# Kernel tuning notes

Hardware: AMD Instinct MI355X
Metric: run time of the kernel (lower is better)

## Reference

```python
import jax, jax.numpy as jnp
import numpy as np

NUM_GROUPS = 32
EPS = 1e-5


def setup_inputs() -> dict:
    key = jax.random.key(0)
    ks = jax.random.split(key, 3)
    B, C, H, W = 4, 256, 64, 64
    x = jax.random.normal(ks[0], (B, C, H, W), dtype=jnp.float32)
    gn_w = jnp.ones((C,), dtype=jnp.float32)
    gn_b = jnp.zeros((C,), dtype=jnp.float32)
    qkv_w = jax.random.normal(ks[1], (3 * C, C), dtype=jnp.float32) * (C ** -0.5)
    qkv_b = jnp.zeros((3 * C,), dtype=jnp.float32)
    proj_w = jax.random.normal(ks[2], (C, C), dtype=jnp.float32) * (C ** -0.5)
    proj_b = jnp.zeros((C,), dtype=jnp.float32)
    return {"x": x, "gn_w": gn_w, "gn_b": gn_b, "qkv_w": qkv_w,
            "qkv_b": qkv_b, "proj_w": proj_w, "proj_b": proj_b}


def group_norm(x, w, b):
    B, C, H, W = x.shape
    xg = x.reshape(B, NUM_GROUPS, C // NUM_GROUPS, H, W)
    mu = xg.mean(axis=(2, 3, 4), keepdims=True)
    var = xg.var(axis=(2, 3, 4), keepdims=True)
    xn = ((xg - mu) * jax.lax.rsqrt(var + EPS)).reshape(B, C, H, W)
    return xn * w[None, :, None, None] + b[None, :, None, None]


def reference(x, gn_w, gn_b, qkv_w, qkv_b, proj_w, proj_b):
    B, C, H, W = x.shape
    h = group_norm(x, gn_w, gn_b)
    # 1x1 conv == per-pixel matmul over channels
    qkv = jnp.einsum('oc,bchw->bohw', qkv_w, h) + qkv_b[None, :, None, None]
    q, k, v = jnp.split(qkv, 3, axis=1)          # each [B, C, H, W]
    q = q.reshape(B, C, H * W).transpose(0, 2, 1)  # [B, N, C]
    k = k.reshape(B, C, H * W)                     # [B, C, N]
    v = v.reshape(B, C, H * W).transpose(0, 2, 1)  # [B, N, C]
    attn = jnp.einsum('bnc,bcm->bnm', q, k) * (C ** -0.5)
    attn = jax.nn.softmax(attn, axis=-1)
    h = jnp.einsum('bnm,bmc->bnc', attn, v)        # [B, N, C]
    h = h.transpose(0, 2, 1).reshape(B, C, H, W)
    out = jnp.einsum('oc,bchw->bohw', proj_w, h) + proj_b[None, :, None, None]
    return x + out
```

## Files before the change

### kernel.cpp

```cpp
#include <hip/hip_runtime.h>
#include <hip/hip_bf16.h>

#define DEVI __device__ __forceinline__

typedef short bf16x8 __attribute__((ext_vector_type(8)));
typedef float f32x4  __attribute__((ext_vector_type(4)));
typedef float f32x16 __attribute__((ext_vector_type(16)));
typedef unsigned short u16;
typedef unsigned int u32;

using bf16 = __hip_bfloat16;

DEVI bf16x8 ld8(const bf16* p) { return *reinterpret_cast<const bf16x8*>(p); }

DEVI u16 f2bu(float f) {
  union { bf16 h; u16 u; } c; c.h = __float2bfloat16(f); return c.u;
}
DEVI float b2f(u16 u) {
  union { float f; unsigned int i; } c; c.i = ((unsigned int)u) << 16; return c.f;
}

DEVI void gload_lds16(const bf16* g, bf16* l) {
  typedef const __attribute__((address_space(1))) char* gp_t;
  typedef __attribute__((address_space(3))) char* lp_t;
  __builtin_amdgcn_global_load_lds((gp_t)(const void*)g, (lp_t)(void*)l, 16, 0, 0);
}

#define MFMA16(a, b, c) __builtin_amdgcn_mfma_f32_16x16x32_bf16((a), (b), (c), 0, 0, 0)
#define MFMA32(a, b, c) __builtin_amdgcn_mfma_f32_32x32x16_bf16((a), (b), (c), 0, 0, 0)


__global__ __launch_bounds__(256) void wconv_kernel(const float* __restrict__ wq,
                                                    const float* __restrict__ wp,
                                                    bf16* __restrict__ wqb,
                                                    bf16* __restrict__ wpb) {
  int tid = blockIdx.x * 256 + threadIdx.x;
  const bool isq = tid < 49152;
  float4 v = isq ? ((const float4*)wq)[tid] : ((const float4*)wp)[tid - 49152];
  alignas(8) bf16 o[4] = { __float2bfloat16(v.x), __float2bfloat16(v.y),
                           __float2bfloat16(v.z), __float2bfloat16(v.w) };
  uint2 pk = *reinterpret_cast<uint2*>(o);
  if (isq) ((uint2*)wqb)[tid] = pk;
  else     ((uint2*)wpb)[tid - 49152] = pk;
}

__global__ __launch_bounds__(256) void gn_kernel(const float* __restrict__ x,
                                                 const float* __restrict__ gw,
                                                 const float* __restrict__ gb,
                                                 bf16* __restrict__ ht) {
  const int blk = blockIdx.x;
  const int bb = blk >> 5, g = blk & 31;
  const float* xg = x + (size_t)(bb * 256 + g * 8) * 4096;

  float s = 0.f, ss = 0.f;
  const float4* x4 = (const float4*)xg;
  for (int i = threadIdx.x; i < 8192; i += 256) {
    float4 v = x4[i];
    s  += v.x + v.y + v.z + v.w;
    ss += v.x * v.x + v.y * v.y + v.z * v.z + v.w * v.w;
  }
  #pragma unroll
  for (int off = 32; off; off >>= 1) {
    s  += __shfl_down(s, off);
    ss += __shfl_down(ss, off);
  }
  __shared__ float red[8];
  int wave = threadIdx.x >> 6;
  if ((threadIdx.x & 63) == 0) { red[wave * 2] = s; red[wave * 2 + 1] = ss; }
  __syncthreads();
  if (threadIdx.x == 0) {
    float S = red[0] + red[2] + red[4] + red[6];
    float SS = red[1] + red[3] + red[5] + red[7];
    float mu = S * (1.f / 32768.f);
    float var = SS * (1.f / 32768.f) - mu * mu;
    red[0] = mu; red[1] = rsqrtf(var + 1e-5f);
  }
  __syncthreads();
  const float mu = red[0], rstd = red[1];

  float gm[8], bt[8];
  #pragma unroll
  for (int j = 0; j < 8; ++j) {
    float wv = gw[g * 8 + j] * rstd;
    gm[j] = wv; bt[j] = gb[g * 8 + j] - mu * wv;
  }
  bf16* hrow = ht + (size_t)bb * 4096 * 256 + g * 8;
  for (int n = threadIdx.x; n < 4096; n += 256) {
    alignas(16) u16 u[8];
    #pragma unroll
    for (int j = 0; j < 8; ++j)
      u[j] = f2bu(xg[j * 4096 + n] * gm[j] + bt[j]);
    *reinterpret_cast<uint4*>(hrow + (size_t)n * 256) = *reinterpret_cast<uint4*>(u);
  }
}

__global__ __launch_bounds__(256, 2) void qkv_gemm(const bf16* __restrict__ ht,
                                                   const bf16* __restrict__ wq,
                                                   const float* __restrict__ qkvb,
                                                   bf16* __restrict__ qkvt) {
  const int phys = blockIdx.x;
  const int L = (phys & 7) * 96 + (phys >> 3);
  const int bb = L / 192; const int rem = L - bb * 192;
  const int nt = rem / 6, ot = rem - nt * 6;

  const int tid = threadIdx.x, lane = tid & 63, w = tid >> 6;
  const int ln = lane & 15, hi = lane >> 4;
  const int wr = w >> 1, wc = w & 1;
  const int n_base = nt * 128, o_base = ot * 128;
  const bf16* hb = ht + (size_t)bb * 4096 * 256;

  __shared__ bf16 At[2][128 * 64];
  __shared__ bf16 Bt[2][128 * 64];

  f32x4 acc[4][4] = {};

  {
    #pragma unroll
    for (int i = 0; i < 4; ++i) {
      int G = i * 256 + tid; int row = G >> 3, g = G & 7;
      int cofs = (g ^ (row & 7)) << 3;
      gload_lds16(hb + (size_t)(n_base + row) * 256 + cofs, At[0] + (size_t)G * 8);
      gload_lds16(wq + (size_t)(o_base + row) * 256 + cofs, Bt[0] + (size_t)G * 8);
    }
  }
  __syncthreads();

  int cur = 0;
  for (int ks = 0; ks < 4; ++ks) {
    if (ks < 3) {
      int k0 = (ks + 1) * 64;
      #pragma unroll
      for (int i = 0; i < 4; ++i) {
        int G = i * 256 + tid; int row = G >> 3, g = G & 7;
        int cofs = k0 + ((g ^ (row & 7)) << 3);
        gload_lds16(hb + (size_t)(n_base + row) * 256 + cofs, At[cur ^ 1] + (size_t)G * 8);
        gload_lds16(wq + (size_t)(o_base + row) * 256 + cofs, Bt[cur ^ 1] + (size_t)G * 8);
      }
    }
    const char* Ab = (const char*)At[cur];
    const char* Bb = (const char*)Bt[cur];
    __builtin_amdgcn_s_setprio(1);
    #pragma unroll
    for (int cb = 0; cb < 2; ++cb) {
      bf16x8 af[4], bfr[4];
      #pragma unroll
      for (int i = 0; i < 4; ++i) {
        int row = wr * 64 + i * 16 + ln;
        af[i] = *(const bf16x8*)(Ab + row * 128 + (((cb * 4 + hi) ^ (row & 7)) << 4));
      }
      #pragma unroll
      for (int j = 0; j < 4; ++j) {
        int row = wc * 64 + j * 16 + ln;
        bfr[j] = *(const bf16x8*)(Bb + row * 128 + (((cb * 4 + hi) ^ (row & 7)) << 4));
      }
      #pragma unroll
      for (int i = 0; i < 4; ++i)
        #pragma unroll
        for (int j = 0; j < 4; ++j)
          acc[i][j] = MFMA16(af[i], bfr[j], acc[i][j]);
    }
    __builtin_amdgcn_s_setprio(0);
    __syncthreads();
    cur ^= 1;
  }

  const float sc = (ot < 2) ? 0.0625f : 1.0f;
  bf16* ob = qkvt + (size_t)bb * 4096 * 768;
  #pragma unroll
  for (int j = 0; j < 4; ++j) {
    int o = o_base + wc * 64 + j * 16 + ln;
    float bias = qkvb[o];
    #pragma unroll
    for (int i = 0; i < 4; ++i)
      #pragma unroll
      for (int r = 0; r < 4; ++r) {
        int n = n_base + wr * 64 + i * 16 + hi * 4 + r;
        ob[(size_t)n * 768 + o] = __float2bfloat16((acc[i][j][r] + bias) * sc);
      }
  }
}

__global__ __launch_bounds__(256) void vtrans_kernel(const bf16* __restrict__ qkvt,
                                                     bf16* __restrict__ vT) {
  int bid = blockIdx.x;
  int ct = bid & 3, ntile = (bid >> 2) & 63, bb = bid >> 8;
  __shared__ bf16 T[64][72];
  int tid = threadIdx.x;
  int i = tid >> 3, j8 = (tid & 7) * 8;
  const bf16* src = qkvt + (size_t)bb * 4096 * 768 + (size_t)(ntile * 64 + i) * 768 + 512 + ct * 64 + j8;
  #pragma unroll
  for (int p = 0; p < 2; ++p) {
    bf16x8 v = ld8(src + (size_t)p * 32 * 768);
    *reinterpret_cast<bf16x8*>(&T[i + p * 32][j8]) = v;
  }
  __syncthreads();
  bf16* dst = vT + (size_t)bb * 256 * 4096 + (size_t)(ct * 64) * 4096 + ntile * 64;
  #pragma unroll
  for (int p = 0; p < 2; ++p) {
    int c = i + p * 32;
    alignas(16) bf16 u[8];
    #pragma unroll
    for (int q = 0; q < 8; ++q) u[q] = T[j8 + q][c];
    *reinterpret_cast<uint4*>(dst + (size_t)c * 4096 + j8) = *reinterpret_cast<uint4*>(u);
  }
}

__global__ __launch_bounds__(256, 2) void attn_kernel(const bf16* __restrict__ qkvt,
                                                      const bf16* __restrict__ vT,
                                                      bf16* __restrict__ Opart,
                                                      float* __restrict__ ml) {
  const int phys = blockIdx.x;
  const int x = phys & 7, c = phys >> 3;
  const int gs = x * 2 + (c >> 5);
  const int qt = c & 31;
  const int bb = gs >> 2, sp = gs & 3;

  const int tid = threadIdx.x, lane = tid & 63, w = tid >> 6;
  const int ln32 = lane & 31, h = lane >> 5;
  const bool h0 = (h == 0);
  const int n0w = qt * 128 + w * 32;

  const bf16* qb = qkvt + (size_t)bb * 4096 * 768;
  const bf16* vb = vT + (size_t)bb * 256 * 4096;

  __shared__ bf16 KT[2][32 * 256];
  __shared__ bf16 VT2[2][256 * 32];

  bf16x8 aq[16];
  #pragma unroll
  for (int step = 0; step < 16; ++step)
    aq[step] = ld8(qb + (size_t)(n0w + ln32) * 768 + step * 16 + h * 8);

  f32x16 acc[8] = {};
  float m_run = -3.0e38f, lsum = 0.f;

  {
    int m0 = sp * 1024;
    #pragma unroll
    for (int i = 0; i < 4; ++i) {
      int G = i * 256 + tid;
      int kr = G >> 5, kc = G & 31;
      gload_lds16(qb + (size_t)(m0 + kr) * 768 + 256 + ((kc ^ kr) << 3), KT[0] + (size_t)G * 8);
      int vr = G >> 2, s = G & 3;
      int gsrc = (s + 4 - (vr >> 1)) & 3;
      gload_lds16(vb + (size_t)vr * 4096 + m0 + (gsrc << 3), VT2[0] + (size_t)G * 8);
    }
  }
  __syncthreads();

  int cur = 0;
  for (int t = 0; t < 32; ++t) {
    if (t < 31) {
      int m0n = sp * 1024 + (t + 1) * 32;
      #pragma unroll
      for (int i = 0; i < 4; ++i) {
        int G = i * 256 + tid;
        int kr = G >> 5, kc = G & 31;
        gload_lds16(qb + (size_t)(m0n + kr) * 768 + 256 + ((kc ^ kr) << 3), KT[cur ^ 1] + (size_t)G * 8);
        int vr = G >> 2, s = G & 3;
        int gsrc = (s + 4 - (vr >> 1)) & 3;
        gload_lds16(vb + (size_t)vr * 4096 + m0n + (gsrc << 3), VT2[cur ^ 1] + (size_t)G * 8);
      }
    }

    const char* Kb = (const char*)KT[cur];
    const char* Vb = (const char*)VT2[cur];

    f32x16 s0 = {};
    __builtin_amdgcn_s_setprio(1);
    #pragma unroll
    for (int step = 0; step < 16; ++step) {
      bf16x8 k0 = *(const bf16x8*)(Kb + ln32 * 512 + (((step * 2 + h) ^ ln32) << 4));
      s0 = MFMA32(k0, aq[step], s0);
    }
    __builtin_amdgcn_s_setprio(0);

    float mx = -3.0e38f;
    #pragma unroll
    for (int r = 0; r < 16; ++r) mx = fmaxf(mx, s0[r]);
    mx = fmaxf(mx, __shfl_xor(mx, 32));

    if (__any(mx > m_run + 8.f)) {
      float mnew = fmaxf(m_run, mx);
      float alpha = __expf(m_run - mnew);
      m_run = mnew;
      lsum *= alpha;
      #pragma unroll
      for (int r = 0; r < 16; ++r) {
        int qacc = (r & 3) + 8 * (r >> 2) + 4 * h;
        float ar = __shfl(alpha, qacc);
        #pragma unroll
        for (int ct = 0; ct < 8; ++ct) acc[ct][r] *= ar;
      }
    }

    u32 pk0[8], sw0[8];
    #pragma unroll
    for (int m = 0; m < 8; ++m) {
      float a0 = __expf(s0[2 * m] - m_run), b0 = __expf(s0[2 * m + 1] - m_run);
      lsum += a0 + b0;
      pk0[m] = ((u32)f2bu(b0) << 16) | f2bu(a0);
    }
    #pragma unroll
    for (int m = 0; m < 8; ++m) sw0[m] = __shfl_xor(pk0[m], 32);

    __builtin_amdgcn_s_setprio(1);
    #pragma unroll
    for (int st = 0; st < 2; ++st) {
      const int A0 = 4 * st, A1 = A0 + 2;
      union { bf16x8 v; u32 u[4]; } af;
      af.u[0] = h0 ? pk0[A0]     : sw0[A1];
      af.u[1] = h0 ? pk0[A0 + 1] : sw0[A1 + 1];
      af.u[2] = h0 ? sw0[A0]     : pk0[A1];
      af.u[3] = h0 ? sw0[A0 + 1] : pk0[A1 + 1];
      #pragma unroll
      for (int ct = 0; ct < 8; ++ct) {
        int vrow = ct * 32 + ln32;
        bf16x8 bv = *(const bf16x8*)(Vb + vrow * 64 + ((((st * 2 + h) + (vrow >> 1)) & 3) << 4));
        acc[ct] = MFMA32(af.v, bv, acc[ct]);
      }
    }
    __builtin_amdgcn_s_setprio(0);

    __syncthreads();
    cur ^= 1;
  }

  float Lrow = lsum + __shfl_xor(lsum, 32);
  size_t rb = (size_t)sp * 16384 + (size_t)bb * 4096;
  if (lane < 32) {
    ml[(rb + n0w + lane) * 2]     = m_run;
    ml[(rb + n0w + lane) * 2 + 1] = Lrow;
  }
  bf16* ob = Opart + rb * 256;
  #pragma unroll
  for (int r = 0; r < 16; ++r) {
    int qacc = (r & 3) + 8 * (r >> 2) + 4 * h;
    int n = n0w + qacc;
    #pragma unroll
    for (int ct = 0; ct < 8; ++ct)
      ob[(size_t)n * 256 + ct * 32 + ln32] = __float2bfloat16(acc[ct][r]);
  }
}

__global__ __launch_bounds__(256) void combine_kernel(const bf16* __restrict__ Opart,
                                                      const float* __restrict__ ml,
                                                      bf16* __restrict__ ho) {
  int rowg = blockIdx.x * 32 + (threadIdx.x >> 3);
  int cg = (threadIdx.x & 7) * 32;
  float msp[4]; float M = -3.0e38f;
  #pragma unroll
  for (int sp = 0; sp < 4; ++sp) {
    msp[sp] = ml[((size_t)sp * 16384 + rowg) * 2];
    M = fmaxf(M, msp[sp]);
  }
  float acc[32];
  #pragma unroll
  for (int j = 0; j < 32; ++j) acc[j] = 0.f;
  float Ltot = 0.f;
  #pragma unroll
  for (int sp = 0; sp < 4; ++sp) {
    float sc = __expf(msp[sp] - M);
    Ltot += ml[((size_t)sp * 16384 + rowg) * 2 + 1] * sc;
    const bf16* p = Opart + ((size_t)sp * 16384 + rowg) * 256 + cg;
    #pragma unroll
    for (int v = 0; v < 4; ++v) {
      bf16x8 u = ld8(p + v * 8);
      #pragma unroll
      for (int j = 0; j < 8; ++j) acc[v * 8 + j] += sc * b2f((u16)u[j]);
    }
  }
  float inv = 1.f / Ltot;
  bf16* o = ho + (size_t)rowg * 256 + cg;
  #pragma unroll
  for (int v = 0; v < 4; ++v) {
    alignas(16) u16 u[8];
    #pragma unroll
    for (int j = 0; j < 8; ++j) u[j] = f2bu(acc[v * 8 + j] * inv);
    *reinterpret_cast<uint4*>(o + v * 8) = *reinterpret_cast<uint4*>(u);
  }
}

__global__ __launch_bounds__(256, 2) void proj_gemm(const bf16* __restrict__ ho,
                                                    const bf16* __restrict__ wp,
                                                    const float* __restrict__ pb,
                                                    const float* __restrict__ x,
                                                    float* __restrict__ out) {
  const int phys = blockIdx.x;
  const int L = (phys & 7) * 32 + (phys >> 3);
  const int bb = L >> 6; const int rem = L & 63;
  const int ot = rem >> 5, nt = rem & 31;

  const int tid = threadIdx.x, lane = tid & 63, w = tid >> 6;
  const int ln = lane & 15, hi = lane >> 4;
  const int wr = w >> 1, wc = w & 1;
  const int o_base = ot * 128, n_base = nt * 128;
  const bf16* hb = ho + (size_t)bb * 4096 * 256;

  __shared__ bf16 Wt[2][128 * 64];
  __shared__ bf16 Ht[2][128 * 64];

  f32x4 acc[4][4] = {};

  {
    #pragma unroll
    for (int i = 0; i < 4; ++i) {
      int G = i * 256 + tid; int row = G >> 3, g = G & 7;
      int cofs = (g ^ (row & 7)) << 3;
      gload_lds16(wp + (size_t)(o_base + row) * 256 + cofs, Wt[0] + (size_t)G * 8);
      gload_lds16(hb + (size_t)(n_base + row) * 256 + cofs, Ht[0] + (size_t)G * 8);
    }
  }
  __syncthreads();

  int cur = 0;
  for (int ks = 0; ks < 4; ++ks) {
    if (ks < 3) {
      int k0 = (ks + 1) * 64;
      #pragma unroll
      for (int i = 0; i < 4; ++i) {
        int G = i * 256 + tid; int row = G >> 3, g = G & 7;
        int cofs = k0 + ((g ^ (row & 7)) << 3);
        gload_lds16(wp + (size_t)(o_base + row) * 256 + cofs, Wt[cur ^ 1] + (size_t)G * 8);
        gload_lds16(hb + (size_t)(n_base + row) * 256 + cofs, Ht[cur ^ 1] + (size_t)G * 8);
      }
    }
    const char* Ab = (const char*)Wt[cur];
    const char* Bb = (const char*)Ht[cur];
    __builtin_amdgcn_s_setprio(1);
    #pragma unroll
    for (int cb = 0; cb < 2; ++cb) {
      bf16x8 af[4], bfr[4];
      #pragma unroll
      for (int i = 0; i < 4; ++i) {
        int row = wr * 64 + i * 16 + ln;
        af[i] = *(const bf16x8*)(Ab + row * 128 + (((cb * 4 + hi) ^ (row & 7)) << 4));
      }
      #pragma unroll
      for (int j = 0; j < 4; ++j) {
        int row = wc * 64 + j * 16 + ln;
        bfr[j] = *(const bf16x8*)(Bb + row * 128 + (((cb * 4 + hi) ^ (row & 7)) << 4));
      }
      #pragma unroll
      for (int i = 0; i < 4; ++i)
        #pragma unroll
        for (int j = 0; j < 4; ++j)
          acc[i][j] = MFMA16(af[i], bfr[j], acc[i][j]);
    }
    __builtin_amdgcn_s_setprio(0);
    __syncthreads();
    cur ^= 1;
  }

  const float* xb = x + (size_t)bb * 256 * 4096;
  float* ob = out + (size_t)bb * 256 * 4096;
  #pragma unroll
  for (int i = 0; i < 4; ++i)
    #pragma unroll
    for (int r = 0; r < 4; ++r) {
      int o = o_base + wr * 64 + i * 16 + hi * 4 + r;
      float bias = pb[o];
      #pragma unroll
      for (int j = 0; j < 4; ++j) {
        int n = n_base + wc * 64 + j * 16 + ln;
        size_t idx = (size_t)o * 4096 + n;
        ob[idx] = xb[idx] + bias + acc[i][j][r];
      }
    }
}

extern "C" void kernel_launch(void* const* d_in, const int* in_sizes, int n_in,
                              void* d_out, int out_size, void* d_ws, size_t ws_size,
                              hipStream_t stream) {
  const float* x   = (const float*)d_in[0];
  const float* gnw = (const float*)d_in[1];
  const float* gnb = (const float*)d_in[2];
  const float* qw  = (const float*)d_in[3];
  const float* qb  = (const float*)d_in[4];
  const float* pw  = (const float*)d_in[5];
  const float* pb  = (const float*)d_in[6];
  float* out = (float*)d_out;

  char* ws = (char*)d_ws;
  bf16* ht    = (bf16*)(ws);
  bf16* qkvt  = (bf16*)(ws + ((size_t)8 << 20));
  bf16* vT    = (bf16*)(ws + ((size_t)32 << 20));
  bf16* ho    = (bf16*)(ws + ((size_t)40 << 20));
  bf16* wqb   = (bf16*)(ws + ((size_t)48 << 20));
  bf16* wpb   = (bf16*)(ws + ((size_t)48 << 20) + 768 * 256 * 2);
  float* ml   = (float*)(ws + ((size_t)48 << 20) + ((size_t)1 << 19));
  bf16* Opart = (bf16*)(ws + ((size_t)49 << 20));

  wconv_kernel<<<dim3(256), dim3(256), 0, stream>>>(qw, pw, wqb, wpb);
  gn_kernel<<<dim3(128), dim3(256), 0, stream>>>(x, gnw, gnb, ht);
  qkv_gemm<<<dim3(768), dim3(256), 0, stream>>>(ht, wqb, qb, qkvt);
  vtrans_kernel<<<dim3(1024), dim3(256), 0, stream>>>(qkvt, vT);
  attn_kernel<<<dim3(512), dim3(256), 0, stream>>>(qkvt, vT, Opart, ml);
  combine_kernel<<<dim3(512), dim3(256), 0, stream>>>(Opart, ml, ho);
  proj_gemm<<<dim3(256), dim3(256), 0, stream>>>(ho, wpb, pb, x, out);
}
```

Measured before the change: 247.6 us.

## Use FP8 for the P·V matmul with a pre-packed FP8 V layout

The V transpose kernel now converts V to FP8 and writes it in a blocked layout that matches the MFMA operand order. The attention kernel loads half as many V bytes into LDS and quantizes the softmax probabilities to FP8, so it can use the fp8 32x32x16 MFMA for P·V. The aim is to cut V bandwidth, LDS traffic and PV MFMA cost. The trade is lower precision in P and V. The rescale threshold also drops from 8 to 6 to keep exponentials within FP8 range.

```diff
diff --git a/kernel.cpp b/kernel.cpp
--- a/kernel.cpp
+++ b/kernel.cpp
@@ -20,14 +20,21 @@
   union { float f; unsigned int i; } c; c.i = ((unsigned int)u) << 16; return c.f;
 }
 
-DEVI void gload_lds16(const bf16* g, bf16* l) {
+DEVI void gload_lds16(const void* g, void* l) {
   typedef const __attribute__((address_space(1))) char* gp_t;
   typedef __attribute__((address_space(3))) char* lp_t;
-  __builtin_amdgcn_global_load_lds((gp_t)(const void*)g, (lp_t)(void*)l, 16, 0, 0);
+  __builtin_amdgcn_global_load_lds((gp_t)g, (lp_t)l, 16, 0, 0);
+}
+
+DEVI u32 pk_fp8(float a, float b, float c, float d) {
+  int t = __builtin_amdgcn_cvt_pk_fp8_f32(a, b, 0, false);
+  t = __builtin_amdgcn_cvt_pk_fp8_f32(c, d, t, true);
+  return (u32)t;
 }
 
 #define MFMA16(a, b, c) __builtin_amdgcn_mfma_f32_16x16x32_bf16((a), (b), (c), 0, 0, 0)
 #define MFMA32(a, b, c) __builtin_amdgcn_mfma_f32_32x32x16_bf16((a), (b), (c), 0, 0, 0)
+#define MFMA32F8(a, b, c) __builtin_amdgcn_mfma_f32_32x32x16_fp8_fp8((a), (b), (c), 0, 0, 0)
 
 
 __global__ __launch_bounds__(256) void wconv_kernel(const float* __restrict__ wq,
@@ -180,8 +187,8 @@
   }
 }
 
-__global__ __launch_bounds__(256) void vtrans_kernel(const bf16* __restrict__ qkvt,
-                                                     bf16* __restrict__ vT) {
+__global__ __launch_bounds__(256) void vfp8_kernel(const bf16* __restrict__ qkvt,
+                                                   unsigned char* __restrict__ vf) {
   int bid = blockIdx.x;
   int ct = bid & 3, ntile = (bid >> 2) & 63, bb = bid >> 8;
   __shared__ bf16 T[64][72];
@@ -194,19 +201,24 @@
     *reinterpret_cast<bf16x8*>(&T[i + p * 32][j8]) = v;
   }
   __syncthreads();
-  bf16* dst = vT + (size_t)bb * 256 * 4096 + (size_t)(ct * 64) * 4096 + ntile * 64;
   #pragma unroll
   for (int p = 0; p < 2; ++p) {
-    int c = i + p * 32;
-    alignas(16) bf16 u[8];
-    #pragma unroll
-    for (int q = 0; q < 8; ++q) u[q] = T[j8 + q][c];
-    *reinterpret_cast<uint4*>(dst + (size_t)c * 4096 + j8) = *reinterpret_cast<uint4*>(u);
+    int u = p * 256 + tid;
+    int cl = u & 63, s = (u >> 6) & 3, k2 = u >> 8;
+    float e[8];
+    #pragma unroll
+    for (int j = 0; j < 8; ++j)
+      e[j] = __bfloat162float(T[k2 * 32 + s * 8 + j][cl]);
+    uint2 pk;
+    pk.x = pk_fp8(e[0], e[1], e[2], e[3]);
+    pk.y = pk_fp8(e[4], e[5], e[6], e[7]);
+    size_t off = (((size_t)(bb * 128 + ntile * 2 + k2) * 4 + s) * 256 + (ct * 64 + cl)) * 8;
+    *reinterpret_cast<uint2*>(vf + off) = pk;
   }
 }
 
 __global__ __launch_bounds__(256, 2) void attn_kernel(const bf16* __restrict__ qkvt,
-                                                      const bf16* __restrict__ vT,
+                                                      const unsigned char* __restrict__ vf,
                                                       bf16* __restrict__ Opart,
                                                       float* __restrict__ ml) {
   const int phys = blockIdx.x;
@@ -221,10 +233,10 @@
   const int n0w = qt * 128 + w * 32;
 
   const bf16* qb = qkvt + (size_t)bb * 4096 * 768;
-  const bf16* vb = vT + (size_t)bb * 256 * 4096;
+  const unsigned char* vb = vf + (size_t)bb * 1048576;
 
   __shared__ bf16 KT[2][32 * 256];
-  __shared__ bf16 VT2[2][256 * 32];
+  __shared__ unsigned char VT2[2][8192];
 
   bf16x8 aq[16];
   #pragma unroll
@@ -236,14 +248,17 @@
 
   {
     int m0 = sp * 1024;
+    const unsigned char* vsrc = vb + (size_t)(sp * 32) * 8192;
     #pragma unroll
     for (int i = 0; i < 4; ++i) {
       int G = i * 256 + tid;
       int kr = G >> 5, kc = G & 31;
       gload_lds16(qb + (size_t)(m0 + kr) * 768 + 256 + ((kc ^ kr) << 3), KT[0] + (size_t)G * 8);
-      int vr = G >> 2, s = G & 3;
-      int gsrc = (s + 4 - (vr >> 1)) & 3;
-      gload_lds16(vb + (size_t)vr * 4096 + m0 + (gsrc << 3), VT2[0] + (size_t)G * 8);
+    }
+    #pragma unroll
+    for (int i = 0; i < 2; ++i) {
+      int G = i * 256 + tid;
+      gload_lds16(vsrc + (size_t)G * 16, VT2[0] + (size_t)G * 16);
     }
   }
   __syncthreads();
@@ -251,15 +266,19 @@
   int cur = 0;
   for (int t = 0; t < 32; ++t) {
     if (t < 31) {
-      int m0n = sp * 1024 + (t + 1) * 32;
+      int kvbn = sp * 32 + t + 1;
+      int m0n = kvbn * 32;
+      const unsigned char* vsrc = vb + (size_t)kvbn * 8192;
       #pragma unroll
       for (int i = 0; i < 4; ++i) {
         int G = i * 256 + tid;
         int kr = G >> 5, kc = G & 31;
         gload_lds16(qb + (size_t)(m0n + kr) * 768 + 256 + ((kc ^ kr) << 3), KT[cur ^ 1] + (size_t)G * 8);
-        int vr = G >> 2, s = G & 3;
-        int gsrc = (s + 4 - (vr >> 1)) & 3;
-        gload_lds16(vb + (size_t)vr * 4096 + m0n + (gsrc << 3), VT2[cur ^ 1] + (size_t)G * 8);
+      }
+      #pragma unroll
+      for (int i = 0; i < 2; ++i) {
+        int G = i * 256 + tid;
+        gload_lds16(vsrc + (size_t)G * 16, VT2[cur ^ 1] + (size_t)G * 16);
       }
     }
 
@@ -280,7 +299,7 @@
     for (int r = 0; r < 16; ++r) mx = fmaxf(mx, s0[r]);
     mx = fmaxf(mx, __shfl_xor(mx, 32));
 
-    if (__any(mx > m_run + 8.f)) {
+    if (__any(mx > m_run + 6.f)) {
       float mnew = fmaxf(m_run, mx);
       float alpha = __expf(m_run - mnew);
       m_run = mnew;
@@ -294,30 +313,29 @@
       }
     }
 
-    u32 pk0[8], sw0[8];
-    #pragma unroll
-    for (int m = 0; m < 8; ++m) {
-      float a0 = __expf(s0[2 * m] - m_run), b0 = __expf(s0[2 * m + 1] - m_run);
-      lsum += a0 + b0;
-      pk0[m] = ((u32)f2bu(b0) << 16) | f2bu(a0);
-    }
-    #pragma unroll
-    for (int m = 0; m < 8; ++m) sw0[m] = __shfl_xor(pk0[m], 32);
+    u32 pq[4], swq[4];
+    #pragma unroll
+    for (int g = 0; g < 4; ++g) {
+      float e0 = __expf(s0[4 * g]     - m_run);
+      float e1 = __expf(s0[4 * g + 1] - m_run);
+      float e2 = __expf(s0[4 * g + 2] - m_run);
+      float e3 = __expf(s0[4 * g + 3] - m_run);
+      lsum += (e0 + e1) + (e2 + e3);
+      pq[g] = pk_fp8(e0, e1, e2, e3);
+    }
+    #pragma unroll
+    for (int g = 0; g < 4; ++g) swq[g] = __shfl_xor(pq[g], 32);
 
     __builtin_amdgcn_s_setprio(1);
     #pragma unroll
     for (int st = 0; st < 2; ++st) {
-      const int A0 = 4 * st, A1 = A0 + 2;
-      union { bf16x8 v; u32 u[4]; } af;
-      af.u[0] = h0 ? pk0[A0]     : sw0[A1];
-      af.u[1] = h0 ? pk0[A0 + 1] : sw0[A1 + 1];
-      af.u[2] = h0 ? sw0[A0]     : pk0[A1];
-      af.u[3] = h0 ? sw0[A0 + 1] : pk0[A1 + 1];
+      union { u32 u[2]; long long l; } a_;
+      a_.u[0] = h0 ? pq[2 * st]  : swq[2 * st + 1];
+      a_.u[1] = h0 ? swq[2 * st] : pq[2 * st + 1];
       #pragma unroll
       for (int ct = 0; ct < 8; ++ct) {
-        int vrow = ct * 32 + ln32;
-        bf16x8 bv = *(const bf16x8*)(Vb + vrow * 64 + ((((st * 2 + h) + (vrow >> 1)) & 3) << 4));
-        acc[ct] = MFMA32(af.v, bv, acc[ct]);
+        long long bvl = *(const long long*)(Vb + (st * 2 + h) * 2048 + (ct * 32 + ln32) * 8);
+        acc[ct] = MFMA32F8(a_.l, bvl, acc[ct]);
       }
     }
     __builtin_amdgcn_s_setprio(0);
@@ -484,7 +502,7 @@
   char* ws = (char*)d_ws;
   bf16* ht    = (bf16*)(ws);
   bf16* qkvt  = (bf16*)(ws + ((size_t)8 << 20));
-  bf16* vT    = (bf16*)(ws + ((size_t)32 << 20));
+  unsigned char* vf = (unsigned char*)(ws + ((size_t)32 << 20));
   bf16* ho    = (bf16*)(ws + ((size_t)40 << 20));
   bf16* wqb   = (bf16*)(ws + ((size_t)48 << 20));
   bf16* wpb   = (bf16*)(ws + ((size_t)48 << 20) + 768 * 256 * 2);
@@ -494,8 +512,8 @@
   wconv_kernel<<<dim3(256), dim3(256), 0, stream>>>(qw, pw, wqb, wpb);
   gn_kernel<<<dim3(128), dim3(256), 0, stream>>>(x, gnw, gnb, ht);
   qkv_gemm<<<dim3(768), dim3(256), 0, stream>>>(ht, wqb, qb, qkvt);
-  vtrans_kernel<<<dim3(1024), dim3(256), 0, stream>>>(qkvt, vT);
-  attn_kernel<<<dim3(512), dim3(256), 0, stream>>>(qkvt, vT, Opart, ml);
+  vfp8_kernel<<<dim3(1024), dim3(256), 0, stream>>>(qkvt, vf);
+  attn_kernel<<<dim3(512), dim3(256), 0, stream>>>(qkvt, vf, Opart, ml);
   combine_kernel<<<dim3(512), dim3(256), 0, stream>>>(Opart, ml, ho);
   proj_gemm<<<dim3(256), dim3(256), 0, stream>>>(ho, wpb, pb, x, out);
 }
```

New measurement: 214.0 us. -13.6%, faster.
